# Optimization experiments

Measured on AMD Instinct MI355X. Metric: run time of the kernel, lower is better.

The kernel has to match this reference:

```python
import jax, jax.numpy as jnp
import numpy as np

HIDDEN = 256

def setup_inputs() -> dict:
    key = jax.random.key(0)
    ks = jax.random.split(key, 8)
    B, T, D, O, H = 128, 1024, 512, 128, HIDDEN
    s_ih = 1.0 / np.sqrt(H)
    inp = {
        "input_x": jax.random.normal(ks[0], (B, T, D), dtype=jnp.float32),
        # PyTorch LSTM params, gate order (i, f, g, o)
        "W_ih": jax.random.uniform(ks[1], (4 * H, D), minval=-s_ih, maxval=s_ih, dtype=jnp.float32),
        "W_hh": jax.random.uniform(ks[2], (4 * H, H), minval=-s_ih, maxval=s_ih, dtype=jnp.float32),
        "b_ih": jax.random.uniform(ks[3], (4 * H,), minval=-s_ih, maxval=s_ih, dtype=jnp.float32),
        "b_hh": jax.random.uniform(ks[4], (4 * H,), minval=-s_ih, maxval=s_ih, dtype=jnp.float32),
        "W_out": jax.random.uniform(ks[5], (O, H), minval=-s_ih, maxval=s_ih, dtype=jnp.float32),
        "b_out": jax.random.uniform(ks[6], (O,), minval=-s_ih, maxval=s_ih, dtype=jnp.float32),
    }
    return inp

def _lstm_last_hidden(input_x, W_ih, W_hh, b_ih, b_hh):
    B, T, D = input_x.shape
    H = HIDDEN
    # Batch the input projection over all timesteps (one big GEMM): [B,T,4H]
    xg = jnp.einsum("btd,gd->btg", input_x, W_ih) + b_ih + b_hh
    xg = jnp.transpose(xg, (1, 0, 2))  # [T,B,4H] for scan over time

    def step(carry, xg_t):
        h, c = carry
        gates = xg_t + h @ W_hh.T  # [B,4H]
        i, f, g, o = jnp.split(gates, 4, axis=-1)
        i = jax.nn.sigmoid(i)
        f = jax.nn.sigmoid(f)
        g = jnp.tanh(g)
        o = jax.nn.sigmoid(o)
        c = f * c + i * g
        h = o * jnp.tanh(c)
        return (h, c), None

    h0 = jnp.zeros((B, H), dtype=input_x.dtype)
    c0 = jnp.zeros((B, H), dtype=input_x.dtype)
    (h_T, _), _ = jax.lax.scan(step, (h0, c0), xg)
    return h_T  # == y[:, -1, :]

def reference(input_x, W_ih, W_hh, b_ih, b_hh, W_out, b_out):
    h_T = _lstm_last_hidden(input_x, W_ih, W_hh, b_ih, b_hh)
    # Dropout is identity in eval mode; squeeze(dim=1) is a no-op for O>1.
    return h_T @ W_out.T + b_out  # [B, O]
```

## Files before the change

### kernel.cpp

```cpp
#include <hip/hip_runtime.h>
#include <hip/hip_bf16.h>

#define B_ 128
#define T_ 1024
#define D_ 512
#define H_ 256
#define G_ 1024

typedef __bf16 bf16_t;
typedef __bf16 bf16x8 __attribute__((ext_vector_type(8)));
typedef __bf16 bf16x4 __attribute__((ext_vector_type(4)));
typedef float  f32x4  __attribute__((ext_vector_type(4)));

__device__ __forceinline__ float fast_rcp(float x) { return __builtin_amdgcn_rcpf(x); }

__device__ __forceinline__ float sigmoid_f(float x) {
  return fast_rcp(1.0f + __expf(-x));
}
__device__ __forceinline__ float tanh_f(float x) {
  x = fminf(fmaxf(x, -15.0f), 15.0f);
  float e = __expf(-2.0f * x);
  return (1.0f - e) * fast_rcp(1.0f + e);
}

__device__ __forceinline__ void barrier_lds_only() {
  asm volatile("s_waitcnt lgkmcnt(0)\n\ts_barrier" ::: "memory");
}

__device__ __forceinline__ void gload_lds16(const void* g, void* l) {
  __builtin_amdgcn_global_load_lds(
      (const __attribute__((address_space(1))) void*)g,
      (__attribute__((address_space(3))) void*)l, 16, 0, 0);
}

__global__ __launch_bounds__(256) void prep_kernel(
    const float* __restrict__ Whh, const float* __restrict__ bih,
    const float* __restrict__ bhh, bf16_t* __restrict__ whhb,
    float* __restrict__ bias) {
  int i = blockIdx.x * 256 + threadIdx.x;
  if (i < G_ * H_) whhb[i] = (bf16_t)Whh[i];
  if (i < G_) bias[i] = bih[i] + bhh[i];
}

__global__ __launch_bounds__(256) void prep_full_kernel(
    const float* __restrict__ Whh, const float* __restrict__ bih,
    const float* __restrict__ bhh, const float* __restrict__ Wih,
    bf16_t* __restrict__ whhb, bf16_t* __restrict__ wihb,
    float* __restrict__ bias) {
  int i = blockIdx.x * 256 + threadIdx.x;
  if (i < G_ * H_) whhb[i] = (bf16_t)Whh[i];
  wihb[i] = (bf16_t)Wih[i];
  if (i < G_) bias[i] = bih[i] + bhh[i];
}

__global__ __launch_bounds__(256) void xconv_kernel(
    const float* __restrict__ X, bf16_t* __restrict__ Xb) {
  const int n4 = (B_ * T_ * D_) / 4;
  const int stride = gridDim.x * 256;
  for (int i = blockIdx.x * 256 + threadIdx.x; i < n4; i += stride) {
    float4 v = ((const float4*)X)[i];
    ((bf16x4*)Xb)[i] =
        (bf16x4){(bf16_t)v.x, (bf16_t)v.y, (bf16_t)v.z, (bf16_t)v.w};
  }
}

__global__ __launch_bounds__(512) void xg_gemm_fast(
    const bf16_t* __restrict__ Xb, const bf16_t* __restrict__ Wihb,
    const float* __restrict__ bias, bf16_t* __restrict__ xg2) {
  __shared__ __align__(16) bf16_t As[128][64];
  __shared__ __align__(16) bf16_t Bs[256][64];

  const int tid = threadIdx.x;
  const int lane = tid & 63;
  const int w = tid >> 6;
  const int q = lane >> 4;
  const int l15 = lane & 15;
  const int m0 = blockIdx.x * 128;
  const int ch0 = blockIdx.y * 64;

  const int lr = lane >> 3;
  const int lc = (lane & 7) * 8;

  f32x4 acc[16];
  #pragma unroll
  for (int n = 0; n < 16; ++n) acc[n] = (f32x4){0.f, 0.f, 0.f, 0.f};

  for (int kt = 0; kt < 8; ++kt) {
    const int k0 = kt * 64;
    __syncthreads();
    #pragma unroll
    for (int j = 0; j < 2; ++j) {
      const int c = w * 2 + j;
      gload_lds16(Xb + (size_t)(m0 + c * 8 + lr) * D_ + k0 + lc,
                  (char*)&As[0][0] + c * 1024);
    }
    #pragma unroll
    for (int j = 0; j < 4; ++j) {
      const int c = w * 4 + j;
      const int br = c * 8 + lr;
      const int wr = (br >> 6) * 256 + ch0 + (br & 63);
      gload_lds16(Wihb + (size_t)wr * D_ + k0 + lc,
                  (char*)&Bs[0][0] + c * 1024);
    }
    __syncthreads();
    #pragma unroll
    for (int kk = 0; kk < 2; ++kk) {
      bf16x8 a = *(const bf16x8*)&As[16 * w + l15][kk * 32 + q * 8];
      #pragma unroll
      for (int n = 0; n < 16; ++n) {
        bf16x8 b = *(const bf16x8*)&Bs[16 * n + l15][kk * 32 + q * 8];
        acc[n] = __builtin_amdgcn_mfma_f32_16x16x32_bf16(a, b, acc[n], 0, 0, 0);
      }
    }
  }
  #pragma unroll
  for (int cs = 0; cs < 4; ++cs) {
    const int cc = ch0 + cs * 16 + l15;
    float bv0 = bias[cc], bv1 = bias[256 + cc];
    float bv2 = bias[512 + cc], bv3 = bias[768 + cc];
    #pragma unroll
    for (int i = 0; i < 4; ++i) {
      int row = m0 + 16 * w + 4 * q + i;
      bf16x4 v = (bf16x4){(bf16_t)(acc[cs][i] + bv0), (bf16_t)(acc[4 + cs][i] + bv1),
                          (bf16_t)(acc[8 + cs][i] + bv2), (bf16_t)(acc[12 + cs][i] + bv3)};
      *(bf16x4*)(xg2 + ((size_t)row * 256 + cc) * 4) = v;
    }
  }
}

__global__ __launch_bounds__(512) void xg_gemm(
    const float* __restrict__ X, const float* __restrict__ Wih,
    const float* __restrict__ bias, bf16_t* __restrict__ xg2) {
  __shared__ __align__(16) bf16_t As[128][72];
  __shared__ __align__(16) bf16_t Bs[256][72];

  const int tid = threadIdx.x;
  const int lane = tid & 63;
  const int w = tid >> 6;
  const int q = lane >> 4;
  const int l15 = lane & 15;
  const int m0 = blockIdx.x * 128;
  const int ch0 = blockIdx.y * 64;

  f32x4 acc[16];
  #pragma unroll
  for (int n = 0; n < 16; ++n) acc[n] = (f32x4){0.f, 0.f, 0.f, 0.f};

  for (int kt = 0; kt < 8; ++kt) {
    const int k0 = kt * 64;
    __syncthreads();
    #pragma unroll
    for (int i = 0; i < 4; ++i) {
      int f = tid + 512 * i;
      int r = f >> 4, c4 = f & 15;
      float4 va = *(const float4*)(X + (size_t)(m0 + r) * D_ + k0 + c4 * 4);
      *(bf16x4*)&As[r][c4 * 4] =
          (bf16x4){(bf16_t)va.x, (bf16_t)va.y, (bf16_t)va.z, (bf16_t)va.w};
    }
    #pragma unroll
    for (int j = 0; j < 8; ++j) {
      int f = tid + 512 * j;
      int r = f >> 4, c4 = f & 15;
      int wr = (r >> 6) * 256 + ch0 + (r & 63);
      float4 vb = *(const float4*)(Wih + (size_t)wr * D_ + k0 + c4 * 4);
      *(bf16x4*)&Bs[r][c4 * 4] =
          (bf16x4){(bf16_t)vb.x, (bf16_t)vb.y, (bf16_t)vb.z, (bf16_t)vb.w};
    }
    __syncthreads();
    #pragma unroll
    for (int kk = 0; kk < 2; ++kk) {
      bf16x8 a = *(const bf16x8*)&As[16 * w + l15][kk * 32 + q * 8];
      #pragma unroll
      for (int n = 0; n < 16; ++n) {
        bf16x8 b = *(const bf16x8*)&Bs[16 * n + l15][kk * 32 + q * 8];
        acc[n] = __builtin_amdgcn_mfma_f32_16x16x32_bf16(a, b, acc[n], 0, 0, 0);
      }
    }
  }
  #pragma unroll
  for (int cs = 0; cs < 4; ++cs) {
    const int cc = ch0 + cs * 16 + l15;
    float bv0 = bias[cc], bv1 = bias[256 + cc];
    float bv2 = bias[512 + cc], bv3 = bias[768 + cc];
    #pragma unroll
    for (int i = 0; i < 4; ++i) {
      int row = m0 + 16 * w + 4 * q + i;
      bf16x4 v = (bf16x4){(bf16_t)(acc[cs][i] + bv0), (bf16_t)(acc[4 + cs][i] + bv1),
                          (bf16_t)(acc[8 + cs][i] + bv2), (bf16_t)(acc[12 + cs][i] + bv3)};
      *(bf16x4*)(xg2 + ((size_t)row * 256 + cc) * 4) = v;
    }
  }
}

__global__ __launch_bounds__(512, 2) void lstm_scan(
    const bf16_t* __restrict__ xg2, const bf16_t* __restrict__ Whh,
    float* __restrict__ hT) {
  __shared__ __align__(16) bf16_t wlds[8 * 16 * 512];
  __shared__ __align__(16) bf16_t hbuf[2][16][264];

  const int tid = threadIdx.x;
  const int lane = tid & 63;
  const int w = tid >> 6;
  const int q = lane >> 4;
  const int l15 = lane & 15;
  const int b0 = blockIdx.x * 8;
  const int rq = (q & 1) * 4 + (q >> 1) * 2;
  const bool hi = (lane >= 32);

  bf16x8 wreg[6][8];
  #pragma unroll
  for (int p2 = 0; p2 < 2; ++p2) {
    #pragma unroll
    for (int g2 = 0; g2 < 4; ++g2) {
      const int j = p2 * 4 + g2;
      const bf16_t* src =
          Whh + (size_t)(g2 * 256 + 32 * w + 16 * p2 + l15) * H_ + q * 8;
      #pragma unroll
      for (int kk = 0; kk < 8; ++kk) {
        bf16x8 v = *(const bf16x8*)(src + kk * 32);
        if (j < 6) {
          wreg[j][kk] = v;
        } else {
          *(bf16x8*)&wlds[(size_t)((w * 16 + (g2 - 2) * 8 + kk)) * 512 + lane * 8] = v;
        }
      }
    }
  }

  for (int i = tid; i < 2 * 16 * 264; i += 512) ((bf16_t*)hbuf)[i] = (bf16_t)0.0f;
  __syncthreads();

  float cst[2][2];
  #pragma unroll
  for (int p = 0; p < 2; ++p) { cst[p][0] = 0.f; cst[p][1] = 0.f; }

  const bf16_t* xp[2][2];
  #pragma unroll
  for (int p = 0; p < 2; ++p)
    #pragma unroll
    for (int k = 0; k < 2; ++k)
      xp[p][k] = xg2 + (size_t)(b0 + rq + k) * (size_t)T_ * 1024 + (32 * w + 16 * p + l15) * 4;

  bf16x4 xv[2][2], xn[2][2];
  #pragma unroll
  for (int p = 0; p < 2; ++p)
    #pragma unroll
    for (int k = 0; k < 2; ++k) {
      xv[p][k] = *(const bf16x4*)xp[p][k];
      xp[p][k] += 1024;
    }

  auto step = [&](int t, bf16x4 (&xc)[2][2], bf16x4 (&xf)[2][2]) {
    #pragma unroll
    for (int p = 0; p < 2; ++p)
      #pragma unroll
      for (int k = 0; k < 2; ++k) {
        xf[p][k] = *(const bf16x4*)xp[p][k];
        xp[p][k] += 1024;
      }
    const int cur = t & 1;
    #pragma unroll
    for (int p = 0; p < 2; ++p) {
      f32x4 acc[4];
      #pragma unroll
      for (int g = 0; g < 4; ++g) acc[g] = (f32x4){0.f, 0.f, 0.f, 0.f};
      #pragma unroll
      for (int kk = 0; kk < 8; ++kk) {
        bf16x8 a = *(const bf16x8*)&hbuf[cur][l15][kk * 32 + q * 8];
        if (p == 0) {
          acc[0] = __builtin_amdgcn_mfma_f32_16x16x32_bf16(a, wreg[0][kk], acc[0], 0, 0, 0);
          acc[1] = __builtin_amdgcn_mfma_f32_16x16x32_bf16(a, wreg[1][kk], acc[1], 0, 0, 0);
          acc[2] = __builtin_amdgcn_mfma_f32_16x16x32_bf16(a, wreg[2][kk], acc[2], 0, 0, 0);
          acc[3] = __builtin_amdgcn_mfma_f32_16x16x32_bf16(a, wreg[3][kk], acc[3], 0, 0, 0);
        } else {
          acc[0] = __builtin_amdgcn_mfma_f32_16x16x32_bf16(a, wreg[4][kk], acc[0], 0, 0, 0);
          acc[1] = __builtin_amdgcn_mfma_f32_16x16x32_bf16(a, wreg[5][kk], acc[1], 0, 0, 0);
          bf16x8 bg = *(const bf16x8*)&wlds[(size_t)(w * 16 + kk) * 512 + lane * 8];
          bf16x8 bo = *(const bf16x8*)&wlds[(size_t)(w * 16 + 8 + kk) * 512 + lane * 8];
          acc[2] = __builtin_amdgcn_mfma_f32_16x16x32_bf16(a, bg, acc[2], 0, 0, 0);
          acc[3] = __builtin_amdgcn_mfma_f32_16x16x32_bf16(a, bo, acc[3], 0, 0, 0);
        }
      }
      float G0[4], G1[4];
      #pragma unroll
      for (int g = 0; g < 4; ++g) {
        float s2 = __shfl(acc[g][2], lane ^ 32, 64);
        float s3 = __shfl(acc[g][3], lane ^ 32, 64);
        G0[g] = hi ? s2 : acc[g][0];
        G1[g] = hi ? s3 : acc[g][1];
      }
      const int c = 32 * w + 16 * p + l15;
      #pragma unroll
      for (int k = 0; k < 2; ++k) {
        const float* Gv_ = k ? G1 : G0;
        float gi = Gv_[0] + (float)xc[p][k][0];
        float gf = Gv_[1] + (float)xc[p][k][1];
        float gg = Gv_[2] + (float)xc[p][k][2];
        float go = Gv_[3] + (float)xc[p][k][3];
        float I = sigmoid_f(gi);
        float F = sigmoid_f(gf);
        float Gg = tanh_f(gg);
        float Ov = sigmoid_f(go);
        float cv = F * cst[p][k] + I * Gg;
        cst[p][k] = cv;
        float hv = Ov * tanh_f(cv);
        hbuf[cur ^ 1][rq + k][c] = (bf16_t)hv;
        if (t == T_ - 1) hT[(size_t)(b0 + rq + k) * H_ + c] = hv;
      }
    }
    barrier_lds_only();
  };

  #pragma unroll 1
  for (int t = 0; t < T_; t += 2) {
    step(t, xv, xn);
    step(t + 1, xn, xv);
  }
}

__global__ __launch_bounds__(128) void head_gemm(
    const float* __restrict__ hT, const float* __restrict__ Wout,
    const float* __restrict__ bout, float* __restrict__ out) {
  __shared__ float hrow[H_];
  const int b = blockIdx.x;
  const int o = threadIdx.x;
  hrow[o] = hT[(size_t)b * H_ + o];
  hrow[o + 128] = hT[(size_t)b * H_ + 128 + o];
  __syncthreads();
  float s = bout[o];
  const float* wr = Wout + (size_t)o * H_;
  #pragma unroll 8
  for (int j = 0; j < H_; ++j) s += hrow[j] * wr[j];
  out[(size_t)b * 128 + o] = s;
}

extern "C" void kernel_launch(void* const* d_in, const int* in_sizes, int n_in,
                              void* d_out, int out_size, void* d_ws, size_t ws_size,
                              hipStream_t stream) {
  const float* X    = (const float*)d_in[0];
  const float* Wih  = (const float*)d_in[1];
  const float* Whh  = (const float*)d_in[2];
  const float* bih  = (const float*)d_in[3];
  const float* bhh  = (const float*)d_in[4];
  const float* Wout = (const float*)d_in[5];
  const float* bout = (const float*)d_in[6];
  float* out = (float*)d_out;

  char* ws = (char*)d_ws;
  const size_t XG_BYTES   = (size_t)B_ * T_ * G_ * 2;
  const size_t WHHB_BYTES = (size_t)G_ * H_ * 2;
  const size_t BIAS_BYTES = (size_t)G_ * 4;
  const size_t HT_BYTES   = (size_t)B_ * H_ * 4;
  const size_t WIHB_BYTES = (size_t)G_ * D_ * 2;
  const size_t XB_BYTES   = (size_t)B_ * T_ * D_ * 2;
  bf16_t* xg2  = (bf16_t*)ws;
  bf16_t* whhb = (bf16_t*)(ws + XG_BYTES);
  float*  bias = (float*)(ws + XG_BYTES + WHHB_BYTES);
  float*  hT   = (float*)(ws + XG_BYTES + WHHB_BYTES + BIAS_BYTES);
  bf16_t* wihb = (bf16_t*)(ws + XG_BYTES + WHHB_BYTES + BIAS_BYTES + HT_BYTES);
  bf16_t* xb   = (bf16_t*)(ws + XG_BYTES + WHHB_BYTES + BIAS_BYTES + HT_BYTES + WIHB_BYTES);

  const size_t NEED_FAST =
      XG_BYTES + WHHB_BYTES + BIAS_BYTES + HT_BYTES + WIHB_BYTES + XB_BYTES;

  if (ws_size >= NEED_FAST) {
    prep_full_kernel<<<dim3(2048), 256, 0, stream>>>(Whh, bih, bhh, Wih, whhb, wihb, bias);
    xconv_kernel<<<dim3(4096), 256, 0, stream>>>(X, xb);
    xg_gemm_fast<<<dim3((B_ * T_) / 128, 4), 512, 0, stream>>>(xb, wihb, bias, xg2);
  } else {
    prep_kernel<<<dim3(1024), 256, 0, stream>>>(Whh, bih, bhh, whhb, bias);
    xg_gemm<<<dim3((B_ * T_) / 128, 4), 512, 0, stream>>>(X, Wih, bias, xg2);
  }
  lstm_scan<<<dim3(B_ / 8), 512, 0, stream>>>(xg2, whhb, hT);
  head_gemm<<<dim3(B_), 128, 0, stream>>>(hT, Wout, bout, out);
}
```

Before: 3.179 ms.

## Retile xg GEMM warps to 2x4 layout with XOR-swizzled LDS reads

Reorganizes the input-projection GEMM so each of 8 warps computes a 64x64 sub-tile (4x4 MFMA fragments) instead of 16 rows by 256 columns. This cuts LDS fragment loads per MFMA, since each A and B fragment is reused four times. An XOR swizzle is applied to the global-to-LDS column placement and to the fragment reads to avoid LDS bank conflicts on the unpadded 64-wide rows. It adds index arithmetic, and the swizzle must match exactly between the store and load sides to stay correct.

```diff
diff --git a/kernel.cpp b/kernel.cpp
--- a/kernel.cpp
+++ b/kernel.cpp
@@ -73,17 +73,25 @@
   const int tid = threadIdx.x;
   const int lane = tid & 63;
   const int w = tid >> 6;
+  const int wm = w >> 2;
+  const int wn = w & 3;
   const int q = lane >> 4;
   const int l15 = lane & 15;
   const int m0 = blockIdx.x * 128;
   const int ch0 = blockIdx.y * 64;
 
   const int lr = lane >> 3;
-  const int lc = (lane & 7) * 8;
-
-  f32x4 acc[16];
-  #pragma unroll
-  for (int n = 0; n < 16; ++n) acc[n] = (f32x4){0.f, 0.f, 0.f, 0.f};
+  const int ls = (lane & 7) ^ (lr & 7);
+  const int lc = ls * 8;
+
+  f32x4 acc[4][4];
+  #pragma unroll
+  for (int mi = 0; mi < 4; ++mi)
+    #pragma unroll
+    for (int nf = 0; nf < 4; ++nf) acc[mi][nf] = (f32x4){0.f, 0.f, 0.f, 0.f};
+
+  const char* As0 = (const char*)&As[0][0];
+  const char* Bs0 = (const char*)&Bs[0][0];
 
   for (int kt = 0; kt < 8; ++kt) {
     const int k0 = kt * 64;
@@ -105,24 +113,37 @@
     __syncthreads();
     #pragma unroll
     for (int kk = 0; kk < 2; ++kk) {
-      bf16x8 a = *(const bf16x8*)&As[16 * w + l15][kk * 32 + q * 8];
-      #pragma unroll
-      for (int n = 0; n < 16; ++n) {
-        bf16x8 b = *(const bf16x8*)&Bs[16 * n + l15][kk * 32 + q * 8];
-        acc[n] = __builtin_amdgcn_mfma_f32_16x16x32_bf16(a, b, acc[n], 0, 0, 0);
-      }
-    }
-  }
-  #pragma unroll
-  for (int cs = 0; cs < 4; ++cs) {
-    const int cc = ch0 + cs * 16 + l15;
-    float bv0 = bias[cc], bv1 = bias[256 + cc];
-    float bv2 = bias[512 + cc], bv3 = bias[768 + cc];
+      bf16x8 a[4], b[4];
+      #pragma unroll
+      for (int mi = 0; mi < 4; ++mi) {
+        const int row = wm * 64 + mi * 16 + l15;
+        a[mi] = *(const bf16x8*)(As0 + row * 128 +
+                                 (((kk * 4 + q) ^ (row & 7)) * 16));
+      }
+      #pragma unroll
+      for (int nf = 0; nf < 4; ++nf) {
+        const int row = nf * 64 + wn * 16 + l15;
+        b[nf] = *(const bf16x8*)(Bs0 + row * 128 +
+                                 (((kk * 4 + q) ^ (row & 7)) * 16));
+      }
+      #pragma unroll
+      for (int mi = 0; mi < 4; ++mi)
+        #pragma unroll
+        for (int nf = 0; nf < 4; ++nf)
+          acc[mi][nf] =
+              __builtin_amdgcn_mfma_f32_16x16x32_bf16(a[mi], b[nf], acc[mi][nf], 0, 0, 0);
+    }
+  }
+  const int cc = ch0 + wn * 16 + l15;
+  const float bv0 = bias[cc], bv1 = bias[256 + cc];
+  const float bv2 = bias[512 + cc], bv3 = bias[768 + cc];
+  #pragma unroll
+  for (int mi = 0; mi < 4; ++mi) {
     #pragma unroll
     for (int i = 0; i < 4; ++i) {
-      int row = m0 + 16 * w + 4 * q + i;
-      bf16x4 v = (bf16x4){(bf16_t)(acc[cs][i] + bv0), (bf16_t)(acc[4 + cs][i] + bv1),
-                          (bf16_t)(acc[8 + cs][i] + bv2), (bf16_t)(acc[12 + cs][i] + bv3)};
+      const int row = m0 + wm * 64 + mi * 16 + 4 * q + i;
+      bf16x4 v = (bf16x4){(bf16_t)(acc[mi][0][i] + bv0), (bf16_t)(acc[mi][1][i] + bv1),
+                          (bf16_t)(acc[mi][2][i] + bv2), (bf16_t)(acc[mi][3][i] + bv3)};
       *(bf16x4*)(xg2 + ((size_t)row * 256 + cc) * 4) = v;
     }
   }
```

Measured after the change: 3.110 ms. 2.2% less time.
